# Performance work log

Hardware: AMD Instinct MI355X
Metric: run time of the kernel (lower is better)

The kernel has to match this reference:

```python
import jax, jax.numpy as jnp
import numpy as np

N_OBJ = 100000
E = 2000000
F_OBJ = 8
NUM_REL = 51


def _linear_params(key, fan_in, fan_out):
    kw, kb = jax.random.split(key)
    bound = 1.0 / np.sqrt(fan_in)
    W = jax.random.uniform(kw, (fan_in, fan_out), jnp.float32, -bound, bound)
    b = jax.random.uniform(kb, (fan_out,), jnp.float32, -bound, bound)
    return W, b


def setup_inputs() -> dict:
    key = jax.random.key(0)
    ks = jax.random.split(key, 10)
    inp = {
        "object_features": jax.random.normal(ks[0], (N_OBJ, F_OBJ), jnp.float32),
        "relations": jax.random.randint(ks[1], (E,), 0, NUM_REL, jnp.int64) if jax.config.jax_enable_x64 else jax.random.randint(ks[1], (E,), 0, NUM_REL, jnp.int32),
        "relation_pairs": jax.random.randint(ks[2], (E, 2), 0, N_OBJ, jnp.int32),
    }
    # object_fc: 16->128->64->32->16 ; relation_fc: 16->8->4->NUM_REL
    dims_obj = [16, 128, 64, 32, 16]
    dims_rel = [16, 8, 4, NUM_REL]
    for i in range(4):
        W, b = _linear_params(ks[3 + i], dims_obj[i], dims_obj[i + 1])
        inp[f"oW{i}"] = W
        inp[f"ob{i}"] = b
    for i in range(3):
        W, b = _linear_params(ks[7 + i], dims_rel[i], dims_rel[i + 1])
        inp[f"rW{i}"] = W
        inp[f"rb{i}"] = b
    return inp


def reference(object_features, relations, relation_pairs,
              oW0, ob0, oW1, ob1, oW2, ob2, oW3, ob3,
              rW0, rb0, rW1, rb1, rW2, rb2):
    # Batched gather over all edges: [E, 16]
    h = jnp.concatenate([object_features[relation_pairs[:, 0]],
                         object_features[relation_pairs[:, 1]]], axis=-1)
    # object_fc: Linear+ReLU x3, final Linear
    h = jax.nn.relu(h @ oW0 + ob0)   # [E,128]
    h = jax.nn.relu(h @ oW1 + ob1)   # [E,64]
    h = jax.nn.relu(h @ oW2 + ob2)   # [E,32]
    h = h @ oW3 + ob3                # [E,16]
    # relation_fc
    h = jax.nn.relu(h @ rW0 + rb0)   # [E,8]
    h = jax.nn.relu(h @ rW1 + rb1)   # [E,4]
    out = h @ rW2 + rb2              # [E,NUM_REL]
    return out, relations
```

## Files before the change

kernel.cpp:

```cpp
#include <hip/hip_runtime.h>


typedef __attribute__((ext_vector_type(8))) short bf16x8;
typedef __attribute__((ext_vector_type(4))) float f32x4;

#define UNROLL _Pragma("unroll")
#define PRIO_HI __builtin_amdgcn_s_setprio(1)
#define PRIO_LO __builtin_amdgcn_s_setprio(0)

__device__ __forceinline__ unsigned fbits(float x) {
    union { float f; unsigned u; } v; v.f = x; return v.u;
}
__device__ __forceinline__ unsigned pk2t(float a, float b) {
    return (fbits(a) >> 16) | (fbits(b) & 0xffff0000u);
}
__device__ __forceinline__ unsigned short bf16rne(float x) {
    unsigned u = fbits(x);
    unsigned r = u + 0x7fffu + ((u >> 16) & 1u);
    return (unsigned short)(r >> 16);
}

__device__ __forceinline__ f32x4 mfma1(bf16x8 a, bf16x8 b, f32x4 acc) {
    return __builtin_amdgcn_mfma_f32_16x16x32_bf16(a, b, acc, 0, 0, 0);
}

__device__ __forceinline__ f32x4 bias4(const float* __restrict__ b, int nt, int g) {
    const float4 v = *(const float4*)(b + nt * 16 + g * 4);
    f32x4 r; r[0] = v.x; r[1] = v.y; r[2] = v.z; r[3] = v.w; return r;
}

__device__ __forceinline__ void chunk_store(unsigned short* __restrict__ tile,
                                            int lr, int klb, f32x4 a) {
    uint2 v; v.x = pk2t(a[0], a[1]); v.y = pk2t(a[2], a[3]);
    const int lanep = lr + 16 * (klb >> 3);
    *(uint2*)(tile + lanep * 8 + (klb & 7)) = v;
}

__device__ __forceinline__ bf16x8 frag_or_const(const unsigned short* __restrict__ tile,
                                                int g, int lid, unsigned k16w) {
    union { bf16x8 v; uint4 u; } t;
    if (g < 2) {
        t.u = *(const uint4*)(tile + lid * 8);
    } else {
        t.u.x = k16w; t.u.y = 0u; t.u.z = 0u; t.u.w = 0u;
    }
    return t.v;
}

__global__ __launch_bounds__(256) void sg_prep(
    const float* __restrict__ oW0, const float* __restrict__ ob0,
    const float* __restrict__ oW1, const float* __restrict__ oW2,
    const float* __restrict__ oW3,
    const float* __restrict__ rW0, const float* __restrict__ rb0,
    const float* __restrict__ rW1, const float* __restrict__ rb1,
    const float* __restrict__ rW2, const float* __restrict__ rb2,
    unsigned short* __restrict__ wsp)
{
    const int idx = blockIdx.x * 256 + threadIdx.x;
    if (idx >= 17920) return;
    if (idx >= 16896) {
        const int t2 = idx - 16896;
        const int tile = t2 >> 9;
        const int l = (t2 >> 3) & 63, j = t2 & 7;
        const int k = (l >> 4) * 8 + j;
        const int n = l & 15;
        float v = 0.0f;
        if (tile == 0) {
            if (n < 8) { if (k < 16) v = rW0[k * 8 + n]; else if (k == 16) v = rb0[n]; }
        } else {
            if (n < 4) { if (k < 8) v = rW1[k * 4 + n]; else if (k == 16) v = rb1[n]; }
        }
        wsp[idx] = bf16rne(v);
        return;
    }
    if (idx >= 14848) {
        const int t2 = idx - 14848;
        const int nt = t2 >> 9;
        const int l = (t2 >> 3) & 63, j = t2 & 7;
        const int k = (l >> 4) * 8 + j;
        const int n = nt * 16 + (l & 15);
        float v = 0.0f;
        if (n < 51) {
            if (k < 4)       v = rW2[k * 51 + n];
            else if (k == 4) v = rb2[n];
        }
        wsp[idx] = bf16rne(v);
        return;
    }
    int t = idx, K, N, kt, nt;
    const float* W;
    bool isW0 = false;
    if (t < 4096)        { W = oW0; K = 16;  N = 128; kt = 0; nt = t >> 9; isW0 = true; }
    else if (t < 12288)  { t -= 4096;  W = oW1; K = 128; N = 64; int f = t >> 9; kt = f >> 2; nt = f & 3; }
    else if (t < 14336)  { t -= 12288; W = oW2; K = 64;  N = 32; int f = t >> 9; kt = f >> 1; nt = f & 1; }
    else                 { t -= 14336; W = oW3; K = 32;  N = 16; kt = 0; nt = 0; }
    const int lid = (t >> 3) & 63, j = t & 7;
    const int k = kt * 32 + (lid >> 4) * 8 + j;
    const int n = nt * 16 + (lid & 15);
    float w = 0.0f;
    if (k < K)                w = W[(size_t)k * N + n];
    else if (isW0 && k == 16) w = ob0[n];
    wsp[idx] = bf16rne(w);
}

__global__ __launch_bounds__(256, 4) void sg_mfma(
    const float* __restrict__ obj, const int* __restrict__ rel,
    const int* __restrict__ pairs,
    const unsigned short* __restrict__ wsp,
    const float* __restrict__ ob1, const float* __restrict__ ob2,
    const float* __restrict__ ob3,
    float* __restrict__ out, float* __restrict__ out_rel, int E)
{
    __shared__ unsigned char smem[24576 + 4 * 4096];
    const int tid = threadIdx.x;
    const int lid = tid & 63;
    const int wid = tid >> 6;
    const int g = lid >> 4, lr = lid & 15;
    unsigned short* wL = (unsigned short*)smem;
    unsigned short* sF = (unsigned short*)(smem + 24576 + wid * 4096);
    const unsigned k16w = (g == 2) ? 0x00003f80u : 0u;

    {
        const uint4* src = (const uint4*)wsp;
        uint4* dst = (uint4*)smem;
        UNROLL for (int i = 0; i < 6; ++i)
            dst[tid + i * 256] = src[tid + i * 256];
    }

    const long long eBase = (long long)blockIdx.x * 256;
    const long long ee = eBase + tid;
    const int e = (ee < E) ? (int)ee : (E - 1);

    {
        const int2 pr = *(const int2*)(pairs + 2 * e);
        const float4* pa = (const float4*)(obj + (size_t)pr.x * 8);
        const float4* pb = (const float4*)(obj + (size_t)pr.y * 8);
        const float4 v0 = pa[0], v1 = pa[1], v2 = pb[0], v3 = pb[1];
        uint4 c0, c1;
        c0.x = pk2t(v0.x, v0.y); c0.y = pk2t(v0.z, v0.w);
        c0.z = pk2t(v1.x, v1.y); c0.w = pk2t(v1.z, v1.w);
        c1.x = pk2t(v2.x, v2.y); c1.y = pk2t(v2.z, v2.w);
        c1.z = pk2t(v3.x, v3.y); c1.w = pk2t(v3.z, v3.w);
        unsigned short* dh = sF + g * 512 + lr * 8;
        *(uint4*)(dh)       = c0;
        *(uint4*)(dh + 128) = c1;
    }

    __syncthreads();

    bf16x8 a0[4];
    UNROLL for (int m = 0; m < 4; ++m)
        a0[m] = frag_or_const(sF + m * 512, g, lid, k16w);

    f32x4 acc2[4][4];
    UNROLL for (int m = 0; m < 4; ++m)
        UNROLL for (int n2 = 0; n2 < 4; ++n2) acc2[m][n2] = bias4(ob1, n2, g);

    const f32x4 z = {0.0f, 0.0f, 0.0f, 0.0f};

    for (int kt2 = 0; kt2 < 4; ++kt2) {
        const bf16x8 w0a = *(const bf16x8*)(wL + (kt2 * 2 + 0) * 512 + lid * 8);
        const bf16x8 w0b = *(const bf16x8*)(wL + (kt2 * 2 + 1) * 512 + lid * 8);
        UNROLL for (int m = 0; m < 4; ++m) {
            f32x4 a = z, b = z;
            PRIO_HI;
            a = mfma1(w0a, a0[m], a);
            b = mfma1(w0b, a0[m], b);
            PRIO_LO;
            UNROLL for (int jr = 0; jr < 4; ++jr) {
                a[jr] = fmaxf(a[jr], 0.0f);
                b[jr] = fmaxf(b[jr], 0.0f);
            }
            chunk_store(sF + m * 512, lr, g * 4, a);
            chunk_store(sF + m * 512, lr, 16 + g * 4, b);
        }
        bf16x8 ah[4];
        UNROLL for (int m = 0; m < 4; ++m)
            ah[m] = *(const bf16x8*)(sF + m * 512 + lid * 8);
        UNROLL for (int n2 = 0; n2 < 4; ++n2) {
            const bf16x8 w = *(const bf16x8*)(wL + 4096 + (kt2 * 4 + n2) * 512 + lid * 8);
            PRIO_HI;
            UNROLL for (int m = 0; m < 4; ++m)
                acc2[m][n2] = mfma1(w, ah[m], acc2[m][n2]);
            PRIO_LO;
        }
    }

    UNROLL for (int m = 0; m < 4; ++m)
        UNROLL for (int n2 = 0; n2 < 4; ++n2)
            UNROLL for (int jr = 0; jr < 4; ++jr)
                acc2[m][n2][jr] = fmaxf(acc2[m][n2][jr], 0.0f);

    f32x4 acc3[4][2];
    UNROLL for (int m = 0; m < 4; ++m)
        UNROLL for (int n3 = 0; n3 < 2; ++n3) acc3[m][n3] = bias4(ob2, n3, g);

    UNROLL for (int kt3 = 0; kt3 < 2; ++kt3) {
        UNROLL for (int m = 0; m < 4; ++m)
            UNROLL for (int ntl = 0; ntl < 2; ++ntl)
                chunk_store(sF + m * 512, lr, ntl * 16 + g * 4, acc2[m][2 * kt3 + ntl]);
        bf16x8 ah3[4];
        UNROLL for (int m = 0; m < 4; ++m)
            ah3[m] = *(const bf16x8*)(sF + m * 512 + lid * 8);
        UNROLL for (int n3 = 0; n3 < 2; ++n3) {
            const bf16x8 w = *(const bf16x8*)(wsp + 12288 + (size_t)(kt3 * 2 + n3) * 512 + lid * 8);
            PRIO_HI;
            UNROLL for (int m = 0; m < 4; ++m)
                acc3[m][n3] = mfma1(w, ah3[m], acc3[m][n3]);
            PRIO_LO;
        }
    }

    UNROLL for (int m = 0; m < 4; ++m) {
        UNROLL for (int n3 = 0; n3 < 2; ++n3) {
            UNROLL for (int jr = 0; jr < 4; ++jr)
                acc3[m][n3][jr] = fmaxf(acc3[m][n3][jr], 0.0f);
            chunk_store(sF + m * 512, lr, n3 * 16 + g * 4, acc3[m][n3]);
        }
    }
    const bf16x8 w4 = *(const bf16x8*)(wsp + 14336 + lid * 8);
    f32x4 acc4[4];
    UNROLL for (int m = 0; m < 4; ++m) {
        bf16x8 ah = *(const bf16x8*)(sF + m * 512 + lid * 8);
        PRIO_HI;
        acc4[m] = mfma1(w4, ah, bias4(ob3, 0, g));
        PRIO_LO;
    }

    const bf16x8 w5 = *(const bf16x8*)(wsp + 16896 + lid * 8);
    const bf16x8 w6 = *(const bf16x8*)(wsp + 17408 + lid * 8);

    UNROLL for (int m = 0; m < 4; ++m)
        chunk_store(sF + m * 512, lr, g * 4, acc4[m]);
    f32x4 acc5[4];
    UNROLL for (int m = 0; m < 4; ++m) {
        bf16x8 b5 = frag_or_const(sF + m * 512, g, lid, k16w);
        PRIO_HI;
        acc5[m] = mfma1(w5, b5, z);
        PRIO_LO;
        UNROLL for (int r = 0; r < 4; ++r) acc5[m][r] = fmaxf(acc5[m][r], 0.0f);
    }

    UNROLL for (int m = 0; m < 4; ++m)
        chunk_store(sF + m * 512, lr, g * 4, acc5[m]);
    f32x4 acc6[4];
    UNROLL for (int m = 0; m < 4; ++m) {
        bf16x8 b6 = frag_or_const(sF + m * 512, g, lid, k16w);
        PRIO_HI;
        acc6[m] = mfma1(w6, b6, z);
        PRIO_LO;
        UNROLL for (int r = 0; r < 4; ++r) acc6[m][r] = fmaxf(acc6[m][r], 0.0f);
    }

    bf16x8 wf[4];
    UNROLL for (int nt = 0; nt < 4; ++nt)
        wf[nt] = *(const bf16x8*)(wsp + 14848 + (size_t)nt * 512 + lid * 8);
    UNROLL for (int mt = 0; mt < 4; ++mt) {
        union { bf16x8 v; uint4 u; } afu;
        afu.u.x = pk2t(acc6[mt][0], acc6[mt][1]);
        afu.u.y = pk2t(acc6[mt][2], acc6[mt][3]);
        afu.u.z = (lid < 16) ? 0x00003f80u : 0u;
        afu.u.w = 0u;
        const long long erow = eBase + (long long)wid * 64 + mt * 16 + g * 4;
        UNROLL for (int nt = 0; nt < 4; ++nt) {
            f32x4 c = z;
            PRIO_HI;
            c = mfma1(afu.v, wf[nt], c);
            PRIO_LO;
            const int colv = nt * 16 + lr;
            UNROLL for (int r = 0; r < 4; ++r) {
                const long long ge = erow + r;
                if (colv < 51 && ge < E) out[ge * 51 + colv] = c[r];
            }
        }
    }

    if (ee < E) out_rel[ee] = (float)rel[e];
}

extern "C" void kernel_launch(void* const* d_in, const int* in_sizes, int n_in,
                              void* d_out, int out_size, void* d_ws, size_t ws_size,
                              hipStream_t stream) {
    const float* obj   = (const float*)d_in[0];
    const int*   rel   = (const int*)  d_in[1];
    const int*   pairs = (const int*)  d_in[2];
    const float* oW0 = (const float*)d_in[3];
    const float* ob0 = (const float*)d_in[4];
    const float* oW1 = (const float*)d_in[5];
    const float* ob1 = (const float*)d_in[6];
    const float* oW2 = (const float*)d_in[7];
    const float* ob2 = (const float*)d_in[8];
    const float* oW3 = (const float*)d_in[9];
    const float* ob3 = (const float*)d_in[10];
    const float* rW0 = (const float*)d_in[11];
    const float* rb0 = (const float*)d_in[12];
    const float* rW1 = (const float*)d_in[13];
    const float* rb1 = (const float*)d_in[14];
    const float* rW2 = (const float*)d_in[15];
    const float* rb2 = (const float*)d_in[16];

    const int E = in_sizes[1];
    float* out     = (float*)d_out;
    float* out_rel = out + (size_t)E * 51;
    unsigned short* wsp = (unsigned short*)d_ws;

    hipLaunchKernelGGL(sg_prep, dim3(70), dim3(256), 0, stream,
                       oW0, ob0, oW1, oW2, oW3,
                       rW0, rb0, rW1, rb1, rW2, rb2, wsp);

    const int blocks = (E + 255) / 256;
    hipLaunchKernelGGL(sg_mfma, dim3(blocks), dim3(256), 0, stream,
                       obj, rel, pairs, wsp,
                       ob1, ob2, ob3,
                       out, out_rel, E);
}
```

Baseline: 185.0 us.

## Make MLP kernel persistent with prefetched next-tile gather, drop setprio

Converts the per-tile kernel into a grid-stride persistent kernel capped at 1024 blocks. Shared-memory weights are loaded once per block instead of once per tile. The random gather for the next tile is issued early so its latency overlaps the MFMA chain of the current tile. The s_setprio hints are also removed. The cost is fewer resident blocks to hide latency and more live registers for the prefetched data.

```diff
diff --git a/kernel.cpp b/kernel.cpp
--- a/kernel.cpp
+++ b/kernel.cpp
@@ -5,8 +5,6 @@
 typedef __attribute__((ext_vector_type(4))) float f32x4;
 
 #define UNROLL _Pragma("unroll")
-#define PRIO_HI __builtin_amdgcn_s_setprio(1)
-#define PRIO_LO __builtin_amdgcn_s_setprio(0)
 
 __device__ __forceinline__ unsigned fbits(float x) {
     union { float f; unsigned u; } v; v.f = x; return v.u;
@@ -119,6 +117,7 @@
     unsigned short* wL = (unsigned short*)smem;
     unsigned short* sF = (unsigned short*)(smem + 24576 + wid * 4096);
     const unsigned k16w = (g == 2) ? 0x00003f80u : 0u;
+    const f32x4 z = {0.0f, 0.0f, 0.0f, 0.0f};
 
     {
         const uint4* src = (const uint4*)wsp;
@@ -126,156 +125,156 @@
         UNROLL for (int i = 0; i < 6; ++i)
             dst[tid + i * 256] = src[tid + i * 256];
     }
-
-    const long long eBase = (long long)blockIdx.x * 256;
-    const long long ee = eBase + tid;
-    const int e = (ee < E) ? (int)ee : (E - 1);
-
-    {
+    __syncthreads();
+
+    const int T = (E + 255) / 256;
+
+    uint4 pc0, pc1;
+    int curE;
+    auto gather = [&](int tt) {
+        const long long ee = (long long)tt * 256 + tid;
+        const int e = (ee < E) ? (int)ee : (E - 1);
         const int2 pr = *(const int2*)(pairs + 2 * e);
         const float4* pa = (const float4*)(obj + (size_t)pr.x * 8);
         const float4* pb = (const float4*)(obj + (size_t)pr.y * 8);
         const float4 v0 = pa[0], v1 = pa[1], v2 = pb[0], v3 = pb[1];
-        uint4 c0, c1;
-        c0.x = pk2t(v0.x, v0.y); c0.y = pk2t(v0.z, v0.w);
-        c0.z = pk2t(v1.x, v1.y); c0.w = pk2t(v1.z, v1.w);
-        c1.x = pk2t(v2.x, v2.y); c1.y = pk2t(v2.z, v2.w);
-        c1.z = pk2t(v3.x, v3.y); c1.w = pk2t(v3.z, v3.w);
-        unsigned short* dh = sF + g * 512 + lr * 8;
-        *(uint4*)(dh)       = c0;
-        *(uint4*)(dh + 128) = c1;
-    }
-
-    __syncthreads();
-
-    bf16x8 a0[4];
-    UNROLL for (int m = 0; m < 4; ++m)
-        a0[m] = frag_or_const(sF + m * 512, g, lid, k16w);
-
-    f32x4 acc2[4][4];
-    UNROLL for (int m = 0; m < 4; ++m)
-        UNROLL for (int n2 = 0; n2 < 4; ++n2) acc2[m][n2] = bias4(ob1, n2, g);
-
-    const f32x4 z = {0.0f, 0.0f, 0.0f, 0.0f};
-
-    for (int kt2 = 0; kt2 < 4; ++kt2) {
-        const bf16x8 w0a = *(const bf16x8*)(wL + (kt2 * 2 + 0) * 512 + lid * 8);
-        const bf16x8 w0b = *(const bf16x8*)(wL + (kt2 * 2 + 1) * 512 + lid * 8);
+        pc0.x = pk2t(v0.x, v0.y); pc0.y = pk2t(v0.z, v0.w);
+        pc0.z = pk2t(v1.x, v1.y); pc0.w = pk2t(v1.z, v1.w);
+        pc1.x = pk2t(v2.x, v2.y); pc1.y = pk2t(v2.z, v2.w);
+        pc1.z = pk2t(v3.x, v3.y); pc1.w = pk2t(v3.z, v3.w);
+        curE = e;
+    };
+
+    gather(blockIdx.x);
+
+    for (int t = blockIdx.x; t < T; t += gridDim.x) {
+        const long long eBase = (long long)t * 256;
+        const long long ee = eBase + tid;
+
+        if (ee < E) out_rel[ee] = (float)rel[curE];
+
+        {
+            unsigned short* dh = sF + g * 512 + lr * 8;
+            *(uint4*)(dh)       = pc0;
+            *(uint4*)(dh + 128) = pc1;
+        }
+
+        bf16x8 a0[4];
+        UNROLL for (int m = 0; m < 4; ++m)
+            a0[m] = frag_or_const(sF + m * 512, g, lid, k16w);
+
+        {
+            const int tn = t + (int)gridDim.x;
+            if (tn < T) gather(tn);
+        }
+
+        f32x4 acc2[4][4];
+        UNROLL for (int m = 0; m < 4; ++m)
+            UNROLL for (int n2 = 0; n2 < 4; ++n2) acc2[m][n2] = bias4(ob1, n2, g);
+
+        for (int kt2 = 0; kt2 < 4; ++kt2) {
+            const bf16x8 w0a = *(const bf16x8*)(wL + (kt2 * 2 + 0) * 512 + lid * 8);
+            const bf16x8 w0b = *(const bf16x8*)(wL + (kt2 * 2 + 1) * 512 + lid * 8);
+            UNROLL for (int m = 0; m < 4; ++m) {
+                f32x4 a = z, b = z;
+                a = mfma1(w0a, a0[m], a);
+                b = mfma1(w0b, a0[m], b);
+                UNROLL for (int jr = 0; jr < 4; ++jr) {
+                    a[jr] = fmaxf(a[jr], 0.0f);
+                    b[jr] = fmaxf(b[jr], 0.0f);
+                }
+                chunk_store(sF + m * 512, lr, g * 4, a);
+                chunk_store(sF + m * 512, lr, 16 + g * 4, b);
+            }
+            bf16x8 ah[4];
+            UNROLL for (int m = 0; m < 4; ++m)
+                ah[m] = *(const bf16x8*)(sF + m * 512 + lid * 8);
+            UNROLL for (int n2 = 0; n2 < 4; ++n2) {
+                const bf16x8 w = *(const bf16x8*)(wL + 4096 + (kt2 * 4 + n2) * 512 + lid * 8);
+                UNROLL for (int m = 0; m < 4; ++m)
+                    acc2[m][n2] = mfma1(w, ah[m], acc2[m][n2]);
+            }
+        }
+
+        UNROLL for (int m = 0; m < 4; ++m)
+            UNROLL for (int n2 = 0; n2 < 4; ++n2)
+                UNROLL for (int jr = 0; jr < 4; ++jr)
+                    acc2[m][n2][jr] = fmaxf(acc2[m][n2][jr], 0.0f);
+
+        f32x4 acc3[4][2];
+        UNROLL for (int m = 0; m < 4; ++m)
+            UNROLL for (int n3 = 0; n3 < 2; ++n3) acc3[m][n3] = bias4(ob2, n3, g);
+
+        UNROLL for (int kt3 = 0; kt3 < 2; ++kt3) {
+            UNROLL for (int m = 0; m < 4; ++m)
+                UNROLL for (int ntl = 0; ntl < 2; ++ntl)
+                    chunk_store(sF + m * 512, lr, ntl * 16 + g * 4, acc2[m][2 * kt3 + ntl]);
+            bf16x8 ah3[4];
+            UNROLL for (int m = 0; m < 4; ++m)
+                ah3[m] = *(const bf16x8*)(sF + m * 512 + lid * 8);
+            UNROLL for (int n3 = 0; n3 < 2; ++n3) {
+                const bf16x8 w = *(const bf16x8*)(wsp + 12288 + (size_t)(kt3 * 2 + n3) * 512 + lid * 8);
+                UNROLL for (int m = 0; m < 4; ++m)
+                    acc3[m][n3] = mfma1(w, ah3[m], acc3[m][n3]);
+            }
+        }
+
         UNROLL for (int m = 0; m < 4; ++m) {
-            f32x4 a = z, b = z;
-            PRIO_HI;
-            a = mfma1(w0a, a0[m], a);
-            b = mfma1(w0b, a0[m], b);
-            PRIO_LO;
-            UNROLL for (int jr = 0; jr < 4; ++jr) {
-                a[jr] = fmaxf(a[jr], 0.0f);
-                b[jr] = fmaxf(b[jr], 0.0f);
-            }
-            chunk_store(sF + m * 512, lr, g * 4, a);
-            chunk_store(sF + m * 512, lr, 16 + g * 4, b);
-        }
-        bf16x8 ah[4];
-        UNROLL for (int m = 0; m < 4; ++m)
-            ah[m] = *(const bf16x8*)(sF + m * 512 + lid * 8);
-        UNROLL for (int n2 = 0; n2 < 4; ++n2) {
-            const bf16x8 w = *(const bf16x8*)(wL + 4096 + (kt2 * 4 + n2) * 512 + lid * 8);
-            PRIO_HI;
-            UNROLL for (int m = 0; m < 4; ++m)
-                acc2[m][n2] = mfma1(w, ah[m], acc2[m][n2]);
-            PRIO_LO;
-        }
-    }
-
-    UNROLL for (int m = 0; m < 4; ++m)
-        UNROLL for (int n2 = 0; n2 < 4; ++n2)
-            UNROLL for (int jr = 0; jr < 4; ++jr)
-                acc2[m][n2][jr] = fmaxf(acc2[m][n2][jr], 0.0f);
-
-    f32x4 acc3[4][2];
-    UNROLL for (int m = 0; m < 4; ++m)
-        UNROLL for (int n3 = 0; n3 < 2; ++n3) acc3[m][n3] = bias4(ob2, n3, g);
-
-    UNROLL for (int kt3 = 0; kt3 < 2; ++kt3) {
-        UNROLL for (int m = 0; m < 4; ++m)
-            UNROLL for (int ntl = 0; ntl < 2; ++ntl)
-                chunk_store(sF + m * 512, lr, ntl * 16 + g * 4, acc2[m][2 * kt3 + ntl]);
-        bf16x8 ah3[4];
-        UNROLL for (int m = 0; m < 4; ++m)
-            ah3[m] = *(const bf16x8*)(sF + m * 512 + lid * 8);
-        UNROLL for (int n3 = 0; n3 < 2; ++n3) {
-            const bf16x8 w = *(const bf16x8*)(wsp + 12288 + (size_t)(kt3 * 2 + n3) * 512 + lid * 8);
-            PRIO_HI;
-            UNROLL for (int m = 0; m < 4; ++m)
-                acc3[m][n3] = mfma1(w, ah3[m], acc3[m][n3]);
-            PRIO_LO;
-        }
-    }
-
-    UNROLL for (int m = 0; m < 4; ++m) {
-        UNROLL for (int n3 = 0; n3 < 2; ++n3) {
-            UNROLL for (int jr = 0; jr < 4; ++jr)
-                acc3[m][n3][jr] = fmaxf(acc3[m][n3][jr], 0.0f);
-            chunk_store(sF + m * 512, lr, n3 * 16 + g * 4, acc3[m][n3]);
-        }
-    }
-    const bf16x8 w4 = *(const bf16x8*)(wsp + 14336 + lid * 8);
-    f32x4 acc4[4];
-    UNROLL for (int m = 0; m < 4; ++m) {
-        bf16x8 ah = *(const bf16x8*)(sF + m * 512 + lid * 8);
-        PRIO_HI;
-        acc4[m] = mfma1(w4, ah, bias4(ob3, 0, g));
-        PRIO_LO;
-    }
-
-    const bf16x8 w5 = *(const bf16x8*)(wsp + 16896 + lid * 8);
-    const bf16x8 w6 = *(const bf16x8*)(wsp + 17408 + lid * 8);
-
-    UNROLL for (int m = 0; m < 4; ++m)
-        chunk_store(sF + m * 512, lr, g * 4, acc4[m]);
-    f32x4 acc5[4];
-    UNROLL for (int m = 0; m < 4; ++m) {
-        bf16x8 b5 = frag_or_const(sF + m * 512, g, lid, k16w);
-        PRIO_HI;
-        acc5[m] = mfma1(w5, b5, z);
-        PRIO_LO;
-        UNROLL for (int r = 0; r < 4; ++r) acc5[m][r] = fmaxf(acc5[m][r], 0.0f);
-    }
-
-    UNROLL for (int m = 0; m < 4; ++m)
-        chunk_store(sF + m * 512, lr, g * 4, acc5[m]);
-    f32x4 acc6[4];
-    UNROLL for (int m = 0; m < 4; ++m) {
-        bf16x8 b6 = frag_or_const(sF + m * 512, g, lid, k16w);
-        PRIO_HI;
-        acc6[m] = mfma1(w6, b6, z);
-        PRIO_LO;
-        UNROLL for (int r = 0; r < 4; ++r) acc6[m][r] = fmaxf(acc6[m][r], 0.0f);
-    }
-
-    bf16x8 wf[4];
-    UNROLL for (int nt = 0; nt < 4; ++nt)
-        wf[nt] = *(const bf16x8*)(wsp + 14848 + (size_t)nt * 512 + lid * 8);
-    UNROLL for (int mt = 0; mt < 4; ++mt) {
-        union { bf16x8 v; uint4 u; } afu;
-        afu.u.x = pk2t(acc6[mt][0], acc6[mt][1]);
-        afu.u.y = pk2t(acc6[mt][2], acc6[mt][3]);
-        afu.u.z = (lid < 16) ? 0x00003f80u : 0u;
-        afu.u.w = 0u;
-        const long long erow = eBase + (long long)wid * 64 + mt * 16 + g * 4;
-        UNROLL for (int nt = 0; nt < 4; ++nt) {
-            f32x4 c = z;
-            PRIO_HI;
-            c = mfma1(afu.v, wf[nt], c);
-            PRIO_LO;
-            const int colv = nt * 16 + lr;
-            UNROLL for (int r = 0; r < 4; ++r) {
-                const long long ge = erow + r;
-                if (colv < 51 && ge < E) out[ge * 51 + colv] = c[r];
-            }
-        }
-    }
-
-    if (ee < E) out_rel[ee] = (float)rel[e];
+            UNROLL for (int n3 = 0; n3 < 2; ++n3) {
+                UNROLL for (int jr = 0; jr < 4; ++jr)
+                    acc3[m][n3][jr] = fmaxf(acc3[m][n3][jr], 0.0f);
+                chunk_store(sF + m * 512, lr, n3 * 16 + g * 4, acc3[m][n3]);
+            }
+        }
+        const bf16x8 w4 = *(const bf16x8*)(wsp + 14336 + lid * 8);
+        f32x4 acc4[4];
+        UNROLL for (int m = 0; m < 4; ++m) {
+            bf16x8 ah = *(const bf16x8*)(sF + m * 512 + lid * 8);
+            acc4[m] = mfma1(w4, ah, bias4(ob3, 0, g));
+        }
+
+        const bf16x8 w5 = *(const bf16x8*)(wsp + 16896 + lid * 8);
+        const bf16x8 w6 = *(const bf16x8*)(wsp + 17408 + lid * 8);
+
+        UNROLL for (int m = 0; m < 4; ++m)
+            chunk_store(sF + m * 512, lr, g * 4, acc4[m]);
+        f32x4 acc5[4];
+        UNROLL for (int m = 0; m < 4; ++m) {
+            bf16x8 b5 = frag_or_const(sF + m * 512, g, lid, k16w);
+            acc5[m] = mfma1(w5, b5, z);
+            UNROLL for (int r = 0; r < 4; ++r) acc5[m][r] = fmaxf(acc5[m][r], 0.0f);
+        }
+
+        UNROLL for (int m = 0; m < 4; ++m)
+            chunk_store(sF + m * 512, lr, g * 4, acc5[m]);
+        f32x4 acc6[4];
+        UNROLL for (int m = 0; m < 4; ++m) {
+            bf16x8 b6 = frag_or_const(sF + m * 512, g, lid, k16w);
+            acc6[m] = mfma1(w6, b6, z);
+            UNROLL for (int r = 0; r < 4; ++r) acc6[m][r] = fmaxf(acc6[m][r], 0.0f);
+        }
+
+        bf16x8 wf[4];
+        UNROLL for (int nt = 0; nt < 4; ++nt)
+            wf[nt] = *(const bf16x8*)(wsp + 14848 + (size_t)nt * 512 + lid * 8);
+        UNROLL for (int mt = 0; mt < 4; ++mt) {
+            union { bf16x8 v; uint4 u; } afu;
+            afu.u.x = pk2t(acc6[mt][0], acc6[mt][1]);
+            afu.u.y = pk2t(acc6[mt][2], acc6[mt][3]);
+            afu.u.z = (lid < 16) ? 0x00003f80u : 0u;
+            afu.u.w = 0u;
+            const long long erow = eBase + (long long)wid * 64 + mt * 16 + g * 4;
+            UNROLL for (int nt = 0; nt < 4; ++nt) {
+                f32x4 c = z;
+                c = mfma1(afu.v, wf[nt], c);
+                const int colv = nt * 16 + lr;
+                UNROLL for (int r = 0; r < 4; ++r) {
+                    const long long ge = erow + r;
+                    if (colv < 51 && ge < E) out[ge * 51 + colv] = c[r];
+                }
+            }
+        }
+    }
 }
 
 extern "C" void kernel_launch(void* const* d_in, const int* in_sizes, int n_in,
@@ -308,7 +307,8 @@
                        oW0, ob0, oW1, oW2, oW3,
                        rW0, rb0, rW1, rb1, rW2, rb2, wsp);
 
-    const int blocks = (E + 255) / 256;
+    const int T = (E + 255) / 256;
+    const int blocks = (T < 1024) ? T : 1024;
     hipLaunchKernelGGL(sg_mfma, dim3(blocks), dim3(256), 0, stream,
                        obj, rel, pairs, wsp,
                        ob1, ob2, ob3,
```

Measured after the change: 320.4 us. 1.73x slower.
